# Kernel optimization log

Hardware: AMD Instinct MI355X
Metric: run time of the kernel (lower is better)

## Reference

```python
import jax, jax.numpy as jnp
import numpy as np
from functools import partial

B, S, D, H, DK, DV, DFF = 4, 2048, 1024, 8, 128, 128, 4096
EPS = 1e-6

def rms_norm(x):
    return x * jax.lax.rsqrt(jnp.mean(x * x, axis=-1, keepdims=True) + EPS)

def l2norm(x):
    return x * jax.lax.rsqrt(jnp.sum(x * x, axis=-1, keepdims=True) + EPS)

def setup_inputs() -> dict:
    key = jax.random.key(0)
    ks = jax.random.split(key, 16)
    w = lambda k, shp: jax.random.normal(k, shp, dtype=jnp.float32) * 0.02
    return {
        'x': jax.random.normal(ks[0], (B, S, D), dtype=jnp.float32),
        'Wq': w(ks[1], (D, H * DK)),
        'Wk': w(ks[2], (D, H * DK)),
        'Wv': w(ks[3], (D, H * DV)),
        'Wb': w(ks[4], (D, H)),
        'Wa': w(ks[5], (D, H)),
        'A_log': jnp.log(jnp.linspace(1.0, 8.0, H).astype(jnp.float32)),
        'dt_bias': jax.random.normal(ks[6], (H,), dtype=jnp.float32) * 0.1,
        'Wg': w(ks[7], (D, H * DV)),
        'o_norm_w': jnp.ones((DV,), dtype=jnp.float32),
        'Wo': w(ks[8], (H * DV, D)),
        'W_fc': w(ks[9], (D, DFF)),
        'W_proj': w(ks[10], (DFF, D)),
    }

def gated_delta_net(h, Wq, Wk, Wv, Wb, Wa, A_log, dt_bias, Wg, o_norm_w, Wo):
    b, s, _ = h.shape
    q = l2norm(jax.nn.silu(h @ Wq).reshape(b, s, H, DK))
    k = l2norm(jax.nn.silu(h @ Wk).reshape(b, s, H, DK))
    v = jax.nn.silu(h @ Wv).reshape(b, s, H, DV)
    beta = jax.nn.sigmoid(h @ Wb)                                  # [b,s,H]
    g = -jnp.exp(A_log) * jax.nn.softplus(h @ Wa + dt_bias)       # [b,s,H]
    alpha = jnp.exp(g)
    scale = DK ** -0.5

    # time-major for scan
    tm = lambda a: jnp.moveaxis(a, 1, 0)
    qs, ks_, vs, als, bts = tm(q), tm(k), tm(v), tm(alpha), tm(beta)

    def step(Sst, inp):
        q_t, k_t, v_t, a_t, b_t = inp               # [b,H,dk],[b,H,dk],[b,H,dv],[b,H],[b,H]
        Sst = Sst * a_t[..., None, None]            # decay state [b,H,dk,dv]
        kv = jnp.einsum('bhd,bhde->bhe', k_t, Sst)  # current memory readout
        delta = (v_t - kv) * b_t[..., None]
        Sst = Sst + jnp.einsum('bhd,bhe->bhde', k_t, delta)
        o_t = jnp.einsum('bhd,bhde->bhe', q_t, Sst) * scale
        return Sst, o_t

    S0 = jnp.zeros((b, H, DK, DV), dtype=h.dtype)
    _, o = jax.lax.scan(step, S0, (qs, ks_, vs, als, bts))
    o = jnp.moveaxis(o, 0, 1)                       # [b,s,H,dv]

    gate = (h @ Wg).reshape(b, s, H, DV)
    o = rms_norm(o) * o_norm_w * jax.nn.silu(gate)  # gated RMSNorm
    return o.reshape(b, s, H * DV) @ Wo

def reference(x, Wq, Wk, Wv, Wb, Wa, A_log, dt_bias, Wg, o_norm_w, Wo, W_fc, W_proj):
    ln_scale = 1.0  # config.layer_norm_scaling = False
    h = gated_delta_net(ln_scale * rms_norm(x), Wq, Wk, Wv, Wb, Wa, A_log, dt_bias, Wg, o_norm_w, Wo)
    x = x + h
    m = ln_scale * rms_norm(x)
    y = jnp.square(jax.nn.relu(m @ W_fc)) @ W_proj  # nanoGPT ReLU^2 MLP
    return x + y
```

## Files before the change

kernel.cpp:

```cpp
#include <hip/hip_runtime.h>
#include <math.h>
#include <stdint.h>

#define ROWS 8192
#define DIM  1024
#define NH   8
#define DFF_ 4096
#define EPSF 1e-6f
#define SCALEQ 0.08838834764831845f

typedef __attribute__((ext_vector_type(8))) short short8;
typedef __attribute__((ext_vector_type(4))) float f32x4;

__device__ __forceinline__ float siluf(float x) {
    float e = __expf(-x);
    return x * __builtin_amdgcn_rcpf(1.0f + e);
}
__device__ __forceinline__ unsigned short f2bf(float f) {
    uint32_t u = __float_as_uint(f);
    uint32_t r = (u + 0x7FFFu + ((u >> 16) & 1u)) >> 16;
    return (unsigned short)r;
}
__device__ __forceinline__ float bf2f(unsigned short u) {
    return __uint_as_float(((uint32_t)u) << 16);
}

__device__ __forceinline__ void async16(const void* g, void* l) {
    __builtin_amdgcn_global_load_lds(
        (const __attribute__((address_space(1))) uint32_t*)g,
        (__attribute__((address_space(3))) uint32_t*)l, 16, 0, 0);
}

__global__ void rmsnorm_bf16_kernel(const float* __restrict__ x, unsigned short* __restrict__ y) {
    int row = blockIdx.x;
    int tid = threadIdx.x;
    const float4* x4 = (const float4*)(x + (size_t)row * DIM);
    float4 v = x4[tid];
    float ss = v.x * v.x + v.y * v.y + v.z * v.z + v.w * v.w;
#pragma unroll
    for (int m = 1; m < 64; m <<= 1) ss += __shfl_xor(ss, m, 64);
    __shared__ float wss[4];
    if ((tid & 63) == 0) wss[tid >> 6] = ss;
    __syncthreads();
    float tot = wss[0] + wss[1] + wss[2] + wss[3];
    float r = rsqrtf(tot * (1.0f / 1024.0f) + EPSF);
    ushort4 o;
    o.x = f2bf(v.x * r); o.y = f2bf(v.y * r); o.z = f2bf(v.z * r); o.w = f2bf(v.w * r);
    ((ushort4*)(y + (size_t)row * DIM))[tid] = o;
}

__global__ void transpose_bf16_kernel(const float* __restrict__ W, unsigned short* __restrict__ WT,
                                      int K, int N) {
    __shared__ float tile[32][33];
    int n0 = blockIdx.x * 32, k0 = blockIdx.y * 32;
    int tx = threadIdx.x & 31, ty = threadIdx.x >> 5;
#pragma unroll
    for (int r = 0; r < 32; r += 8)
        tile[ty + r][tx] = W[(size_t)(k0 + ty + r) * N + n0 + tx];
    __syncthreads();
#pragma unroll
    for (int r = 0; r < 32; r += 8)
        WT[(size_t)(n0 + ty + r) * K + k0 + tx] = f2bf(tile[tx][ty + r]);
}

__global__ void transpose5_kernel(const float* __restrict__ s0, const float* __restrict__ s1,
                                  const float* __restrict__ s2, const float* __restrict__ s3,
                                  const float* __restrict__ s4, unsigned short* __restrict__ dst) {
    __shared__ float tile[32][33];
    int z = blockIdx.z;
    const float* W = (z == 0) ? s0 : (z == 1) ? s1 : (z == 2) ? s2 : (z == 3) ? s3 : s4;
    unsigned short* WT = dst + (size_t)z * (1u << 20);
    int n0 = blockIdx.x * 32, k0 = blockIdx.y * 32;
    int tx = threadIdx.x & 31, ty = threadIdx.x >> 5;
#pragma unroll
    for (int r = 0; r < 32; r += 8)
        tile[ty + r][tx] = W[(size_t)(k0 + ty + r) * 1024 + n0 + tx];
    __syncthreads();
#pragma unroll
    for (int r = 0; r < 32; r += 8)
        WT[(size_t)(n0 + ty + r) * 1024 + k0 + tx] = f2bf(tile[tx][ty + r]);
}

#define G256_DECL \
    __shared__ __align__(16) unsigned short AL[2][2][256 * 32]; \
    __shared__ __align__(16) unsigned short BL[2][2][256 * 32]; \
    int tid = threadIdx.x; \
    int w = tid >> 6, lane = tid & 63; \
    int wm = w >> 2, wn = w & 3; \
    int lr = lane & 15; \
    int nwgx = gridDim.x; \
    int nwg = nwgx * gridDim.y; \
    int id = blockIdx.y * nwgx + blockIdx.x; \
    int cpx = nwg >> 3; \
    int nid = (id & 7) * cpx + (id >> 3); \
    int bxs = nid % nwgx, bys = nid / nwgx; \
    int bm = bys * 256, bn = bxs * 256; \
    int stg_r = w * 32 + (lane >> 2); \
    int stg_c = ((lane & 3) ^ ((lane >> 3) & 3)) * 8; \
    const unsigned short* Ag = A + (size_t)(bm + stg_r) * K + stg_c; \
    const unsigned short* Bg = BT + (size_t)(bn + stg_r) * K + stg_c; \
    int pc = ((lane >> 4) ^ ((lr >> 1) & 3)) * 8; \
    f32x4 acc[8][4] = {}; \
    short8 bf[4], af[4]; \
    int nt = K / 64;

#define G256_STAGE_A(buf, s, kto) do { \
    async16(Ag + (kto) + (s) * 32, &AL[buf][s][(w * 2 + 0) * 512]); \
    async16(Ag + (size_t)16 * K + (kto) + (s) * 32, &AL[buf][s][(w * 2 + 1) * 512]); \
} while (0)
#define G256_STAGE_B(buf, s, kto) do { \
    async16(Bg + (kto) + (s) * 32, &BL[buf][s][(w * 2 + 0) * 512]); \
    async16(Bg + (size_t)16 * K + (kto) + (s) * 32, &BL[buf][s][(w * 2 + 1) * 512]); \
} while (0)

#define G256_READ_B(cur, s) do { \
    _Pragma("unroll") \
    for (int j = 0; j < 4; ++j) \
        bf[j] = *(const short8*)&BL[cur][s][(wn * 64 + j * 16 + lr) * 32 + pc]; \
} while (0)
#define G256_READ_A(cur, s, rh) do { \
    _Pragma("unroll") \
    for (int i = 0; i < 4; ++i) \
        af[i] = *(const short8*)&AL[cur][s][(wm * 128 + (rh) * 64 + i * 16 + lr) * 32 + pc]; \
} while (0)

#define G256_MFMA(rh) do { \
    __builtin_amdgcn_s_barrier(); \
    asm volatile("s_waitcnt lgkmcnt(0)" ::: "memory"); \
    __builtin_amdgcn_s_setprio(1); \
    _Pragma("unroll") \
    for (int i = 0; i < 4; ++i) \
        _Pragma("unroll") \
        for (int j = 0; j < 4; ++j) \
            acc[(rh) * 4 + i][j] = __builtin_amdgcn_mfma_f32_16x16x32_bf16(af[i], bf[j], acc[(rh) * 4 + i][j], 0, 0, 0); \
    __builtin_amdgcn_s_setprio(0); \
} while (0)

#define G256_MAINLOOP \
    G256_STAGE_A(0, 0, 0); G256_STAGE_B(0, 0, 0); \
    G256_STAGE_A(0, 1, 0); G256_STAGE_B(0, 1, 0); \
    asm volatile("s_waitcnt vmcnt(0)" ::: "memory"); \
    __builtin_amdgcn_s_barrier(); \
    for (int t = 0; t < nt; ++t) { \
        int cur = t & 1, nxt = cur ^ 1; \
        bool pf = (t + 1 < nt); \
        int ktn = (t + 1) * 64; \
        G256_READ_B(cur, 0); \
        G256_READ_A(cur, 0, 0); \
        if (pf) G256_STAGE_A(nxt, 0, ktn); \
        G256_MFMA(0); \
        __builtin_amdgcn_s_barrier(); \
        G256_READ_A(cur, 0, 1); \
        if (pf) G256_STAGE_B(nxt, 0, ktn); \
        G256_MFMA(1); \
        asm volatile("s_waitcnt vmcnt(4)" ::: "memory"); \
        __builtin_amdgcn_s_barrier(); \
        G256_READ_B(cur, 1); \
        G256_READ_A(cur, 1, 0); \
        if (pf) G256_STAGE_A(nxt, 1, ktn); \
        G256_MFMA(0); \
        __builtin_amdgcn_s_barrier(); \
        G256_READ_A(cur, 1, 1); \
        if (pf) G256_STAGE_B(nxt, 1, ktn); \
        G256_MFMA(1); \
        asm volatile("s_waitcnt vmcnt(4)" ::: "memory"); \
        __builtin_amdgcn_s_barrier(); \
    }

template <int EPI, typename CT>
__global__ __launch_bounds__(512, 2) void gemm256(
    const unsigned short* __restrict__ A, const unsigned short* __restrict__ BT,
    CT* __restrict__ C, const float* __restrict__ res, int M, int N, int K) {
    G256_DECL
    G256_MAINLOOP

#pragma unroll
    for (int rf = 0; rf < 8; ++rf) {
        int gr0 = bm + wm * 128 + rf * 16 + (lane >> 4) * 4;
#pragma unroll
        for (int cf = 0; cf < 4; ++cf) {
            int gc = bn + wn * 64 + cf * 16 + lr;
#pragma unroll
            for (int r = 0; r < 4; ++r) {
                float v = acc[rf][cf][r];
                size_t idx = (size_t)(gr0 + r) * N + gc;
                if (EPI == 2) v += res[idx];
                else if (EPI == 3) { float t = fmaxf(v, 0.0f); v = t * t; }
                if constexpr (sizeof(CT) == 2) C[idx] = (CT)f2bf(v);
                else C[idx] = v;
            }
        }
    }
}

__global__ __launch_bounds__(512, 2) void qkvg256(
    const unsigned short* __restrict__ A, const unsigned short* __restrict__ BT,
    unsigned short* __restrict__ oq, unsigned short* __restrict__ ok,
    unsigned short* __restrict__ ov, unsigned short* __restrict__ og, int M, int K) {
    __shared__ float sums[256 * 4];
    G256_DECL
    G256_MAINLOOP

    int bsel = bn >> 10;
    int bnl = bn & 1023;
    if (bsel < 3) {
#pragma unroll
        for (int rf = 0; rf < 8; ++rf)
#pragma unroll
            for (int cf = 0; cf < 4; ++cf)
#pragma unroll
                for (int r = 0; r < 4; ++r)
                    acc[rf][cf][r] = siluf(acc[rf][cf][r]);
    }
    bool donorm = (bsel < 2);
    if (donorm) {
#pragma unroll
        for (int rf = 0; rf < 8; ++rf) {
#pragma unroll
            for (int r = 0; r < 4; ++r) {
                float p = acc[rf][0][r] * acc[rf][0][r] + acc[rf][1][r] * acc[rf][1][r] +
                          acc[rf][2][r] * acc[rf][2][r] + acc[rf][3][r] * acc[rf][3][r];
                p += __shfl_xor(p, 1, 16);
                p += __shfl_xor(p, 2, 16);
                p += __shfl_xor(p, 4, 16);
                p += __shfl_xor(p, 8, 16);
                if (lr == 0)
                    sums[(wm * 128 + rf * 16 + (lane >> 4) * 4 + r) * 4 + wn] = p;
            }
        }
        __syncthreads();
    }
    unsigned short* C = (bsel == 0) ? oq : (bsel == 1) ? ok : (bsel == 2) ? ov : og;
#pragma unroll
    for (int rf = 0; rf < 8; ++rf) {
#pragma unroll
        for (int r = 0; r < 4; ++r) {
            int lrow = wm * 128 + rf * 16 + (lane >> 4) * 4 + r;
            float rn = 1.0f;
            if (donorm)
                rn = rsqrtf(sums[lrow * 4 + (wn & 2)] + sums[lrow * 4 + (wn & 2) + 1] + EPSF);
            size_t gr = (size_t)(bm + lrow) * 1024;
#pragma unroll
            for (int cf = 0; cf < 4; ++cf) {
                int gc = bnl + wn * 64 + cf * 16 + lr;
                C[gr + gc] = f2bf(acc[rf][cf][r] * rn);
            }
        }
    }
}

template <int EPI>
__global__ __launch_bounds__(512, 2) void gemm128n(
    const unsigned short* __restrict__ A, const unsigned short* __restrict__ BT,
    float* __restrict__ C, const float* __restrict__ res, int M, int N, int K) {
    __shared__ __align__(16) unsigned short AL[2][2][128 * 32];
    __shared__ __align__(16) unsigned short BL[2][2][256 * 32];
    int tid = threadIdx.x;
    int w = tid >> 6, lane = tid & 63;
    int wm = w >> 2, wn = w & 3;
    int lr = lane & 15;
    int nwgx = gridDim.x;
    int nwg = nwgx * gridDim.y;
    int id = blockIdx.y * nwgx + blockIdx.x;
    int cpx = nwg >> 3;
    int nid = (id & 7) * cpx + (id >> 3);
    int bxs = nid % nwgx, bys = nid / nwgx;
    int bm = bys * 128, bn = bxs * 256;
    int stg_r = w * 16 + (lane >> 2);
    int stg_c = ((lane & 3) ^ ((lane >> 3) & 3)) * 8;
    const unsigned short* Ag = A + (size_t)(bm + stg_r) * K + stg_c;
    const unsigned short* Bg = BT + (size_t)(bn + stg_r) * K + stg_c;
    int pc = ((lane >> 4) ^ ((lr >> 1) & 3)) * 8;
    f32x4 acc[4][4] = {};
    short8 bf[4], af[4];
    int nt = K / 64;

#define G128_STAGE_A(buf, s, kto) \
    async16(Ag + (kto) + (s) * 32, &AL[buf][s][w * 512])
#define G128_STAGE_B(buf, s, kto) do { \
    async16(Bg + (kto) + (s) * 32, &BL[buf][s][w * 512]); \
    async16(Bg + (size_t)128 * K + (kto) + (s) * 32, &BL[buf][s][4096 + w * 512]); \
} while (0)
#define G128_READ(cur, s) do { \
    _Pragma("unroll") \
    for (int j = 0; j < 4; ++j) \
        bf[j] = *(const short8*)&BL[cur][s][(wn * 64 + j * 16 + lr) * 32 + pc]; \
    _Pragma("unroll") \
    for (int i = 0; i < 4; ++i) \
        af[i] = *(const short8*)&AL[cur][s][(wm * 64 + i * 16 + lr) * 32 + pc]; \
} while (0)
#define G128_MFMA() do { \
    __builtin_amdgcn_s_barrier(); \
    asm volatile("s_waitcnt lgkmcnt(0)" ::: "memory"); \
    __builtin_amdgcn_s_setprio(1); \
    _Pragma("unroll") \
    for (int i = 0; i < 4; ++i) \
        _Pragma("unroll") \
        for (int j = 0; j < 4; ++j) \
            acc[i][j] = __builtin_amdgcn_mfma_f32_16x16x32_bf16(af[i], bf[j], acc[i][j], 0, 0, 0); \
    __builtin_amdgcn_s_setprio(0); \
} while (0)

    G128_STAGE_A(0, 0, 0); G128_STAGE_B(0, 0, 0);
    G128_STAGE_A(0, 1, 0); G128_STAGE_B(0, 1, 0);
    asm volatile("s_waitcnt vmcnt(0)" ::: "memory");
    __builtin_amdgcn_s_barrier();
    for (int t = 0; t < nt; ++t) {
        int cur = t & 1, nxt = cur ^ 1;
        bool pf = (t + 1 < nt);
        int ktn = (t + 1) * 64;
        G128_READ(cur, 0);
        if (pf) { G128_STAGE_A(nxt, 0, ktn); G128_STAGE_B(nxt, 0, ktn); }
        G128_MFMA();
        asm volatile("s_waitcnt vmcnt(3)" ::: "memory");
        __builtin_amdgcn_s_barrier();
        G128_READ(cur, 1);
        if (pf) { G128_STAGE_A(nxt, 1, ktn); G128_STAGE_B(nxt, 1, ktn); }
        G128_MFMA();
        asm volatile("s_waitcnt vmcnt(3)" ::: "memory");
        __builtin_amdgcn_s_barrier();
    }

#pragma unroll
    for (int i = 0; i < 4; ++i) {
        int gr0 = bm + wm * 64 + i * 16 + (lane >> 4) * 4;
#pragma unroll
        for (int j = 0; j < 4; ++j) {
            int gc = bn + wn * 64 + j * 16 + lr;
#pragma unroll
            for (int r = 0; r < 4; ++r) {
                float v = acc[i][j][r];
                size_t idx = (size_t)(gr0 + r) * N + gc;
                if (EPI == 2) v += res[idx];
                C[idx] = v;
            }
        }
    }
#undef G128_STAGE_A
#undef G128_STAGE_B
#undef G128_READ
#undef G128_MFMA
}

__global__ void gating_kernel(const float* __restrict__ o, const unsigned short* __restrict__ gate,
                              const float* __restrict__ w, unsigned short* __restrict__ ob) {
    int row = blockIdx.x;
    int tid = threadIdx.x;
    const float4* op = (const float4*)(o + (size_t)row * DIM);
    float4 v = op[tid];
    float ss = v.x * v.x + v.y * v.y + v.z * v.z + v.w * v.w;
#pragma unroll
    for (int m = 1; m < 32; m <<= 1) ss += __shfl_xor(ss, m, 32);
    float r = rsqrtf(ss * (1.0f / 128.0f) + EPSF);
    ushort4 gu = ((const ushort4*)(gate + (size_t)row * DIM))[tid];
    float4 wv = ((const float4*)w)[tid & 31];
    ushort4 out;
    out.x = f2bf(v.x * r * wv.x * siluf(bf2f(gu.x)));
    out.y = f2bf(v.y * r * wv.y * siluf(bf2f(gu.y)));
    out.z = f2bf(v.z * r * wv.z * siluf(bf2f(gu.z)));
    out.w = f2bf(v.w * r * wv.w * siluf(bf2f(gu.w)));
    ((ushort4*)(ob + (size_t)row * DIM))[tid] = out;
}

__global__ void smallproj_kernel(const unsigned short* __restrict__ hbuf,
                                 const float* __restrict__ Wb, const float* __restrict__ Wa,
                                 const float* __restrict__ A_log, const float* __restrict__ dt_bias,
                                 float* __restrict__ Glog, float* __restrict__ Beta) {
    int row = blockIdx.x;
    int tid = threadIdx.x;
    __shared__ __align__(16) float hrow[1024];
    __shared__ float part[128];
    const ushort4* h4 = (const ushort4*)(hbuf + (size_t)row * DIM);
    ushort4 u0 = h4[tid * 2], u1 = h4[tid * 2 + 1];
    hrow[tid * 8 + 0] = bf2f(u0.x); hrow[tid * 8 + 1] = bf2f(u0.y);
    hrow[tid * 8 + 2] = bf2f(u0.z); hrow[tid * 8 + 3] = bf2f(u0.w);
    hrow[tid * 8 + 4] = bf2f(u1.x); hrow[tid * 8 + 5] = bf2f(u1.y);
    hrow[tid * 8 + 6] = bf2f(u1.z); hrow[tid * 8 + 7] = bf2f(u1.w);
    __syncthreads();
    int out = tid & 15, slice = tid >> 4;
    const float* W = (out < 8) ? Wb : Wa;
    int col = out & 7;
    int k0 = slice * 128;
    float p = 0.0f;
    for (int kk = 0; kk < 128; kk++) p += hrow[k0 + kk] * W[(size_t)(k0 + kk) * 8 + col];
    part[tid] = p;
    __syncthreads();
    if (tid < 16) {
        float sum = 0.0f;
#pragma unroll
        for (int sl = 0; sl < 8; sl++) sum += part[sl * 16 + tid];
        if (tid < 8) {
            Beta[(size_t)row * 8 + tid] = 1.0f / (1.0f + expf(-sum));
        } else {
            int hh = tid - 8;
            float xg = sum + dt_bias[hh];
            float sp = fmaxf(xg, 0.0f) + log1pf(expf(-fabsf(xg)));
            Glog[(size_t)row * 8 + hh] = -expf(A_log[hh]) * sp;
        }
    }
}

#define PRE_KB 0
#define PRE_QB 17408
#define PRE_YL 17408
#define PRE_LM 34816
#define PRE_MT 44032
#define PRE_FL 76800
#define PRE_SZ 77824

__global__ __launch_bounds__(256) void chunk_prep_kernel(
    const unsigned short* __restrict__ Q16, const unsigned short* __restrict__ K16,
    const unsigned short* __restrict__ V16, const float* __restrict__ Glog,
    const float* __restrict__ Beta,
    unsigned short* __restrict__ Wg, unsigned short* __restrict__ Ug,
    unsigned short* __restrict__ Qg, unsigned short* __restrict__ KTg,
    unsigned short* __restrict__ SMg, float* __restrict__ Pcs) {
    __shared__ __align__(16) unsigned char smem[PRE_SZ];
    unsigned short* Kb = (unsigned short*)(smem + PRE_KB);
    unsigned short* Qb = (unsigned short*)(smem + PRE_QB);
    unsigned short* Yl = (unsigned short*)(smem + PRE_YL);
    unsigned short* Lm = (unsigned short*)(smem + PRE_LM);
    float* betl = (float*)(smem + PRE_FL);
    float* Gl = betl + 64;
    float* Pl = Gl + 64;
    float* decf = Pl + 64;

    int blk = blockIdx.x;
    int bh = blk & 31, c = blk >> 5;
    int b = bh >> 3, h = bh & 7;
    int bhc = bh * 32 + c;
    int row0 = b * 2048 + c * 64;
    int col0 = h * 128;
    int tid = threadIdx.x;
    int wv = tid >> 6, lane = tid & 63;
    int lr = lane & 15, lk8 = (lane >> 4) * 8, l4 = (lane >> 4) * 4;

#pragma unroll
    for (int r = 0; r < 4; ++r) {
        int cc = tid + r * 256;
        int i = cc >> 4, jc = (cc & 15) * 8;
        *(short8*)&Kb[i * 136 + jc] = *(const short8*)(K16 + (size_t)(row0 + i) * DIM + col0 + jc);
        *(short8*)&Qb[i * 136 + jc] = *(const short8*)(Q16 + (size_t)(row0 + i) * DIM + col0 + jc);
    }
    {
        short8 z = {};
        for (int o = tid; o < 576; o += 256) ((short8*)Lm)[o] = z;
        for (int o = tid; o < 2048; o += 256) ((short8*)(smem + PRE_MT))[o] = z;
    }
    if (tid < 64) {
        float g = Glog[(size_t)(row0 + tid) * 8 + h];
        betl[tid] = Beta[(size_t)(row0 + tid) * 8 + h];
#pragma unroll
        for (int d = 1; d < 64; d <<= 1) {
            float t = __shfl_up(g, d, 64);
            if (tid >= d) g += t;
        }
        Gl[tid] = g;
        Pl[tid] = __expf(g);
        float g63 = __shfl(g, 63, 64);
        decf[tid] = __expf(g63 - g);
        if (tid == 63) Pcs[bhc] = __expf(g);
    }
    __syncthreads();

    for (int nt = 0; nt <= wv; nt++) {
        f32x4 acc = {};
#pragma unroll
        for (int kk = 0; kk < 4; kk++) {
            short8 af = *(const short8*)&Kb[(wv * 16 + lr) * 136 + kk * 32 + lk8];
            short8 bfr = *(const short8*)&Kb[(nt * 16 + lr) * 136 + kk * 32 + lk8];
            acc = __builtin_amdgcn_mfma_f32_16x16x32_bf16(af, bfr, acc, 0, 0, 0);
        }
#pragma unroll
        for (int r = 0; r < 4; r++) {
            int i = wv * 16 + l4 + r;
            int j = nt * 16 + lr;
            if (j < i) Lm[i * 72 + j] = f2bf(betl[i] * __expf(Gl[i] - Gl[j]) * acc[r]);
        }
    }
    for (int nt = 0; nt < 4; nt++) {
        f32x4 acc = {};
        if (nt <= wv) {
#pragma unroll
            for (int kk = 0; kk < 4; kk++) {
                short8 af = *(const short8*)&Qb[(wv * 16 + lr) * 136 + kk * 32 + lk8];
                short8 bfr = *(const short8*)&Kb[(nt * 16 + lr) * 136 + kk * 32 + lk8];
                acc = __builtin_amdgcn_mfma_f32_16x16x32_bf16(af, bfr, acc, 0, 0, 0);
            }
        }
#pragma unroll
        for (int r = 0; r < 4; r++) {
            int i = wv * 16 + l4 + r;
            int j = nt * 16 + lr;
            float vv = (nt <= wv && j <= i) ? SCALEQ * __expf(Gl[i] - Gl[j]) * acc[r] : 0.f;
            SMg[((size_t)bhc * 64 + i) * 64 + j] = f2bf(vv);
        }
    }
    {
        int d = tid & 127, ih = tid >> 7;
        for (int i0 = 0; i0 < 32; i0++) {
            int i = ih * 32 + i0;
            Qg[((size_t)bhc * 64 + i) * 128 + d] = f2bf(SCALEQ * Pl[i] * bf2f(Qb[i * 136 + d]));
        }
        for (int j8 = 0; j8 < 32; j8 += 8) {
            short8 v8;
#pragma unroll
            for (int e = 0; e < 8; e++) {
                int jj = ih * 32 + j8 + e;
                v8[e] = (short)f2bf(decf[jj] * bf2f(Kb[jj * 136 + d]));
            }
            *(short8*)&KTg[((size_t)bhc * 128 + d) * 64 + ih * 32 + j8] = v8;
        }
    }
    __syncthreads();

    int n = tid;
    bool isW = n < 128;
    int cW = n & 127;
    unsigned short* Gout = isW ? Wg : Ug;
    const unsigned short* Vcol = V16 + (size_t)row0 * DIM + col0 + cW;
    for (int bi = 0; bi < 4; ++bi) {
        if (bi > 0) {
            int ib = bi * 16;
#pragma unroll
            for (int t4 = 0; t4 < 4; ++t4) {
                int nt = wv * 4 + t4;
                f32x4 acc = {};
#pragma unroll
                for (int ks = 0; ks < 2; ++ks) {
                    short8 af = *(const short8*)&Lm[(ib + lr) * 72 + ks * 32 + lk8];
                    int nr = nt * 16 + lr;
                    int cj = ks * 4 + (lk8 >> 3);
                    short8 bfr = *(const short8*)(smem + PRE_MT + nr * 128 + (((cj ^ (nr & 7)) & 7) << 4));
                    acc = __builtin_amdgcn_mfma_f32_16x16x32_bf16(af, bfr, acc, 0, 0, 0);
                }
#pragma unroll
                for (int r = 0; r < 4; ++r)
                    Yl[(l4 + r) * 264 + nt * 16 + lr] = f2bf(acc[r]);
            }
        }
        __syncthreads();
        float xs[16];
#pragma unroll
        for (int ii = 0; ii < 16; ++ii) {
            int i = bi * 16 + ii;
            float a = isW ? betl[i] * Pl[i] * bf2f(Kb[i * 136 + cW])
                          : betl[i] * bf2f(Vcol[(size_t)i * DIM]);
            if (bi > 0) a -= bf2f(Yl[ii * 264 + n]);
#pragma unroll
            for (int j = 0; j < 15; ++j)
                if (j < ii) a = fmaf(-bf2f(Lm[i * 72 + bi * 16 + j]), xs[j], a);
            xs[ii] = a;
        }
        {
            short8 m0, m1;
#pragma unroll
            for (int e = 0; e < 8; ++e) { m0[e] = (short)f2bf(xs[e]); m1[e] = (short)f2bf(xs[8 + e]); }
            int cj0 = bi * 2, cj1 = bi * 2 + 1;
            *(short8*)(smem + PRE_MT + n * 128 + (((cj0 ^ (n & 7)) & 7) << 4)) = m0;
            *(short8*)(smem + PRE_MT + n * 128 + (((cj1 ^ (n & 7)) & 7) << 4)) = m1;
        }
#pragma unroll
        for (int ii = 0; ii < 16; ++ii)
            Gout[((size_t)bhc * 64 + bi * 16 + ii) * 128 + cW] = f2bf(xs[ii]);
        __syncthreads();
    }
}

__global__ __launch_bounds__(256) void chunk_scan2_kernel(
    const unsigned short* __restrict__ Wg, const unsigned short* __restrict__ Ug,
    const unsigned short* __restrict__ Qg, const unsigned short* __restrict__ KTg,
    const unsigned short* __restrict__ SMg, const float* __restrict__ Pcs,
    float* __restrict__ O) {
    int blk = blockIdx.x;
    int bh = blk & 31, dvg = blk >> 5;
    int b = bh >> 3, h = bh & 7;
    int col16 = dvg * 16;
    int tid = threadIdx.x;
    int wv = tid >> 6, lane = tid & 63;
    int lr = lane & 15, lk8 = (lane >> 4) * 8, l4 = (lane >> 4) * 4;
    int i0 = wv * 16;

    __shared__ __align__(16) unsigned short Wl[64 * 136];
    __shared__ __align__(16) unsigned short Ql[64 * 136];
    __shared__ __align__(16) unsigned short KTl[128 * 72];
    __shared__ __align__(16) unsigned short SMl[64 * 72];
    __shared__ __align__(16) unsigned short Ul[64 * 24];
    __shared__ __align__(16) unsigned short STl[16 * 136];
    __shared__ __align__(16) unsigned short DTl[16 * 72];

    for (int e = tid; e < 16 * 136; e += 256) STl[e] = 0;

    f32x4 Sacc[2] = {};

    for (int c = 0; c < 32; c++) {
        int bhc = bh * 32 + c;
        size_t base8k = (size_t)bhc * 8192;
        float pc = Pcs[bhc];
#pragma unroll
        for (int r = 0; r < 4; r++) {
            int v = tid + r * 256;
            *(short8*)&Wl[(v >> 4) * 136 + (v & 15) * 8] = *(const short8*)(Wg + base8k + (size_t)v * 8);
            *(short8*)&Ql[(v >> 4) * 136 + (v & 15) * 8] = *(const short8*)(Qg + base8k + (size_t)v * 8);
            *(short8*)&KTl[(v >> 3) * 72 + (v & 7) * 8] = *(const short8*)(KTg + base8k + (size_t)v * 8);
        }
#pragma unroll
        for (int r = 0; r < 2; r++) {
            int v = tid + r * 256;
            *(short8*)&SMl[(v >> 3) * 72 + (v & 7) * 8] = *(const short8*)(SMg + (size_t)bhc * 4096 + (size_t)v * 8);
        }
        if (tid < 128) {
            int row = tid >> 1, hf = tid & 1;
            *(short8*)&Ul[row * 24 + hf * 8] =
                *(const short8*)(Ug + base8k + (size_t)row * 128 + col16 + hf * 8);
        }
        __syncthreads();

        f32x4 acc0 = {}, acc1 = {};
#pragma unroll
        for (int kd = 0; kd < 4; kd++) {
            short8 bfs = *(const short8*)&STl[lr * 136 + kd * 32 + lk8];
            short8 aw = *(const short8*)&Wl[(i0 + lr) * 136 + kd * 32 + lk8];
            short8 aq = *(const short8*)&Ql[(i0 + lr) * 136 + kd * 32 + lk8];
            acc0 = __builtin_amdgcn_mfma_f32_16x16x32_bf16(aw, bfs, acc0, 0, 0, 0);
            acc1 = __builtin_amdgcn_mfma_f32_16x16x32_bf16(aq, bfs, acc1, 0, 0, 0);
        }
        ushort4 dpk;
        dpk.x = f2bf(bf2f(Ul[(i0 + l4 + 0) * 24 + lr]) - acc0[0]);
        dpk.y = f2bf(bf2f(Ul[(i0 + l4 + 1) * 24 + lr]) - acc0[1]);
        dpk.z = f2bf(bf2f(Ul[(i0 + l4 + 2) * 24 + lr]) - acc0[2]);
        dpk.w = f2bf(bf2f(Ul[(i0 + l4 + 3) * 24 + lr]) - acc0[3]);
        *(ushort4*)&DTl[lr * 72 + i0 + l4] = dpk;
        __syncthreads();

#pragma unroll
        for (int dt = 0; dt < 2; dt++)
#pragma unroll
            for (int r = 0; r < 4; r++) Sacc[dt][r] *= pc;
#pragma unroll
        for (int kj = 0; kj < 2; kj++) {
            short8 bfd = *(const short8*)&DTl[lr * 72 + kj * 32 + lk8];
            short8 as = *(const short8*)&SMl[(i0 + lr) * 72 + kj * 32 + lk8];
            acc1 = __builtin_amdgcn_mfma_f32_16x16x32_bf16(as, bfd, acc1, 0, 0, 0);
#pragma unroll
            for (int dt = 0; dt < 2; dt++) {
                short8 ak = *(const short8*)&KTl[((2 * wv + dt) * 16 + lr) * 72 + kj * 32 + lk8];
                Sacc[dt] = __builtin_amdgcn_mfma_f32_16x16x32_bf16(ak, bfd, Sacc[dt], 0, 0, 0);
            }
        }
        {
            int orow0 = b * 2048 + c * 64 + i0 + l4;
            int ocol = h * 128 + col16 + lr;
#pragma unroll
            for (int r = 0; r < 4; r++)
                O[(size_t)(orow0 + r) * DIM + ocol] = acc1[r];
        }
#pragma unroll
        for (int dt = 0; dt < 2; dt++) {
            ushort4 sp;
            sp.x = f2bf(Sacc[dt][0]);
            sp.y = f2bf(Sacc[dt][1]);
            sp.z = f2bf(Sacc[dt][2]);
            sp.w = f2bf(Sacc[dt][3]);
            *(ushort4*)&STl[lr * 136 + (2 * wv + dt) * 16 + l4] = sp;
        }
        __syncthreads();
    }
}

extern "C" void kernel_launch(void* const* d_in, const int* in_sizes, int n_in,
                              void* d_out, int out_size, void* d_ws, size_t ws_size,
                              hipStream_t stream) {
    const float* x      = (const float*)d_in[0];
    const float* Wq     = (const float*)d_in[1];
    const float* Wk     = (const float*)d_in[2];
    const float* Wv     = (const float*)d_in[3];
    const float* Wb     = (const float*)d_in[4];
    const float* Wa     = (const float*)d_in[5];
    const float* A_log  = (const float*)d_in[6];
    const float* dt_b   = (const float*)d_in[7];
    const float* Wg_in  = (const float*)d_in[8];
    const float* o_norm = (const float*)d_in[9];
    const float* Wo     = (const float*)d_in[10];
    const float* W_fc   = (const float*)d_in[11];
    const float* W_proj = (const float*)d_in[12];
    float* out = (float*)d_out;

    const size_t MATE = (size_t)ROWS * DIM;
    unsigned short* qb16 = (unsigned short*)d_ws;
    unsigned short* kb16 = qb16 + MATE;
    unsigned short* vb16 = kb16 + MATE;
    unsigned short* gt16 = vb16 + MATE;
    float* o_f = (float*)(gt16 + MATE);
    unsigned short* h_bf = (unsigned short*)(o_f + MATE);
    float* glog = (float*)(h_bf + MATE);
    float* beta = glog + (size_t)ROWS * NH;
    unsigned short* wts = (unsigned short*)(beta + (size_t)ROWS * NH);
    unsigned short* WqT = wts;
    unsigned short* WoT = wts + 4 * (1u << 20);
    unsigned short* WfcT = wts + 5 * (1u << 20);
    unsigned short* WprT = wts + 9 * (1u << 20);
    unsigned short* Wgb = wts + 13 * (1u << 20);
    unsigned short* Ugb = Wgb + (8u << 20);
    unsigned short* Qg2 = Ugb + (8u << 20);
    unsigned short* KTg = Qg2 + (8u << 20);
    unsigned short* SMg = KTg + (8u << 20);
    float* pcs = (float*)(SMg + (4u << 20));
    unsigned short* m_bf = h_bf;
    unsigned short* o_bf = vb16;
    unsigned short* fc_bf = qb16;

    transpose5_kernel<<<dim3(32, 32, 5), 256, 0, stream>>>(Wq, Wk, Wv, Wg_in, Wo, WqT);
    transpose_bf16_kernel<<<dim3(128, 32), 256, 0, stream>>>(W_fc, WfcT, 1024, 4096);
    transpose_bf16_kernel<<<dim3(32, 128), 256, 0, stream>>>(W_proj, WprT, 4096, 1024);

    rmsnorm_bf16_kernel<<<ROWS, 256, 0, stream>>>(x, h_bf);

    qkvg256<<<dim3(4096 / 256, ROWS / 256), 512, 0, stream>>>(
        h_bf, WqT, qb16, kb16, vb16, gt16, ROWS, DIM);

    smallproj_kernel<<<ROWS, 128, 0, stream>>>(h_bf, Wb, Wa, A_log, dt_b, glog, beta);

    chunk_prep_kernel<<<1024, 256, 0, stream>>>(qb16, kb16, vb16, glog, beta,
                                                Wgb, Ugb, Qg2, KTg, SMg, pcs);
    chunk_scan2_kernel<<<256, 256, 0, stream>>>(Wgb, Ugb, Qg2, KTg, SMg, pcs, o_f);

    gating_kernel<<<ROWS, 256, 0, stream>>>(o_f, gt16, o_norm, o_bf);

    gemm128n<2><<<dim3(1024 / 256, ROWS / 128), 512, 0, stream>>>(
        o_bf, WoT, out, x, ROWS, DIM, DIM);

    rmsnorm_bf16_kernel<<<ROWS, 256, 0, stream>>>(out, m_bf);

    gemm256<3, unsigned short><<<dim3(DFF_ / 256, ROWS / 256), 512, 0, stream>>>(
        m_bf, WfcT, fc_bf, nullptr, ROWS, DFF_, DIM);

    gemm128n<2><<<dim3(1024 / 256, ROWS / 128), 512, 0, stream>>>(
        fc_bf, WprT, out, out, ROWS, DIM, DFF_);
}
```

Baseline: 486.5 us.

## Restructure gemm128n pipeline to one barrier per 64-wide K tile

Reorganizes the gemm128n shared-memory layout from two 32-wide K sub-stages to a single 64-wide row with XOR swizzle over 8 chunks. Each iteration now issues all prefetch loads for the next tile, reads both K halves of fragments, and runs 32 MFMAs before a single wait and barrier. This cuts barrier and wait count per K tile and gives more MFMA work between syncs. The price is more fragment registers. The launch bound also drops the 2-blocks-per-CU hint, which may lower occupancy.

```diff
diff --git a/kernel.cpp b/kernel.cpp
--- a/kernel.cpp
+++ b/kernel.cpp
@@ -250,11 +250,11 @@
 }
 
 template <int EPI>
-__global__ __launch_bounds__(512, 2) void gemm128n(
+__global__ __launch_bounds__(512) void gemm128n(
     const unsigned short* __restrict__ A, const unsigned short* __restrict__ BT,
     float* __restrict__ C, const float* __restrict__ res, int M, int N, int K) {
-    __shared__ __align__(16) unsigned short AL[2][2][128 * 32];
-    __shared__ __align__(16) unsigned short BL[2][2][256 * 32];
+    __shared__ __align__(16) unsigned short AL[2][128 * 64];
+    __shared__ __align__(16) unsigned short BL[2][256 * 64];
     int tid = threadIdx.x;
     int w = tid >> 6, lane = tid & 63;
     int wm = w >> 2, wn = w & 3;
@@ -266,60 +266,62 @@
     int nid = (id & 7) * cpx + (id >> 3);
     int bxs = nid % nwgx, bys = nid / nwgx;
     int bm = bys * 128, bn = bxs * 256;
-    int stg_r = w * 16 + (lane >> 2);
-    int stg_c = ((lane & 3) ^ ((lane >> 3) & 3)) * 8;
-    const unsigned short* Ag = A + (size_t)(bm + stg_r) * K + stg_c;
-    const unsigned short* Bg = BT + (size_t)(bn + stg_r) * K + stg_c;
-    int pc = ((lane >> 4) ^ ((lr >> 1) & 3)) * 8;
+
+    int arow = tid >> 3;
+    int ac = ((tid & 7) ^ (arow & 7)) * 8;
+    const unsigned short* Aga = A + (size_t)(bm + arow) * K + ac;
+    const unsigned short* Bga = BT + (size_t)(bn + arow) * K + ac;
+
+    int pc0 = ((0 * 4 + (lane >> 4)) ^ (lr & 7)) * 8;
+    int pc1 = ((1 * 4 + (lane >> 4)) ^ (lr & 7)) * 8;
+
     f32x4 acc[4][4] = {};
-    short8 bf[4], af[4];
+    short8 af0[4], af1[4], bf0[4], bf1[4];
     int nt = K / 64;
 
-#define G128_STAGE_A(buf, s, kto) \
-    async16(Ag + (kto) + (s) * 32, &AL[buf][s][w * 512])
-#define G128_STAGE_B(buf, s, kto) do { \
-    async16(Bg + (kto) + (s) * 32, &BL[buf][s][w * 512]); \
-    async16(Bg + (size_t)128 * K + (kto) + (s) * 32, &BL[buf][s][4096 + w * 512]); \
+#define G128_STAGE(buf, kto) do { \
+    async16(Aga + (kto), &AL[buf][tid * 8]); \
+    async16(Aga + (size_t)64 * K + (kto), &AL[buf][(512 + tid) * 8]); \
+    async16(Bga + (kto), &BL[buf][tid * 8]); \
+    async16(Bga + (size_t)64 * K + (kto), &BL[buf][(512 + tid) * 8]); \
+    async16(Bga + (size_t)128 * K + (kto), &BL[buf][(1024 + tid) * 8]); \
+    async16(Bga + (size_t)192 * K + (kto), &BL[buf][(1536 + tid) * 8]); \
 } while (0)
-#define G128_READ(cur, s) do { \
-    _Pragma("unroll") \
-    for (int j = 0; j < 4; ++j) \
-        bf[j] = *(const short8*)&BL[cur][s][(wn * 64 + j * 16 + lr) * 32 + pc]; \
-    _Pragma("unroll") \
-    for (int i = 0; i < 4; ++i) \
-        af[i] = *(const short8*)&AL[cur][s][(wm * 64 + i * 16 + lr) * 32 + pc]; \
-} while (0)
-#define G128_MFMA() do { \
-    __builtin_amdgcn_s_barrier(); \
-    asm volatile("s_waitcnt lgkmcnt(0)" ::: "memory"); \
-    __builtin_amdgcn_s_setprio(1); \
-    _Pragma("unroll") \
-    for (int i = 0; i < 4; ++i) \
-        _Pragma("unroll") \
-        for (int j = 0; j < 4; ++j) \
-            acc[i][j] = __builtin_amdgcn_mfma_f32_16x16x32_bf16(af[i], bf[j], acc[i][j], 0, 0, 0); \
-    __builtin_amdgcn_s_setprio(0); \
-} while (0)
-
-    G128_STAGE_A(0, 0, 0); G128_STAGE_B(0, 0, 0);
-    G128_STAGE_A(0, 1, 0); G128_STAGE_B(0, 1, 0);
+
+    G128_STAGE(0, 0);
     asm volatile("s_waitcnt vmcnt(0)" ::: "memory");
     __builtin_amdgcn_s_barrier();
     for (int t = 0; t < nt; ++t) {
         int cur = t & 1, nxt = cur ^ 1;
-        bool pf = (t + 1 < nt);
-        int ktn = (t + 1) * 64;
-        G128_READ(cur, 0);
-        if (pf) { G128_STAGE_A(nxt, 0, ktn); G128_STAGE_B(nxt, 0, ktn); }
-        G128_MFMA();
-        asm volatile("s_waitcnt vmcnt(3)" ::: "memory");
+        if (t + 1 < nt) G128_STAGE(nxt, (t + 1) * 64);
+#pragma unroll
+        for (int i = 0; i < 4; ++i) {
+            af0[i] = *(const short8*)&AL[cur][(wm * 64 + i * 16 + lr) * 64 + pc0];
+            af1[i] = *(const short8*)&AL[cur][(wm * 64 + i * 16 + lr) * 64 + pc1];
+        }
+#pragma unroll
+        for (int j = 0; j < 4; ++j) {
+            bf0[j] = *(const short8*)&BL[cur][(wn * 64 + j * 16 + lr) * 64 + pc0];
+            bf1[j] = *(const short8*)&BL[cur][(wn * 64 + j * 16 + lr) * 64 + pc1];
+        }
+        asm volatile("s_waitcnt lgkmcnt(0)" ::: "memory");
+        __builtin_amdgcn_sched_barrier(0);
+        __builtin_amdgcn_s_setprio(1);
+#pragma unroll
+        for (int i = 0; i < 4; ++i)
+#pragma unroll
+            for (int j = 0; j < 4; ++j)
+                acc[i][j] = __builtin_amdgcn_mfma_f32_16x16x32_bf16(af0[i], bf0[j], acc[i][j], 0, 0, 0);
+#pragma unroll
+        for (int i = 0; i < 4; ++i)
+#pragma unroll
+            for (int j = 0; j < 4; ++j)
+                acc[i][j] = __builtin_amdgcn_mfma_f32_16x16x32_bf16(af1[i], bf1[j], acc[i][j], 0, 0, 0);
+        __builtin_amdgcn_s_setprio(0);
+        asm volatile("s_waitcnt vmcnt(0)" ::: "memory");
         __builtin_amdgcn_s_barrier();
-        G128_READ(cur, 1);
-        if (pf) { G128_STAGE_A(nxt, 1, ktn); G128_STAGE_B(nxt, 1, ktn); }
-        G128_MFMA();
-        asm volatile("s_waitcnt vmcnt(3)" ::: "memory");
-        __builtin_amdgcn_s_barrier();
-    }
+    }
+#undef G128_STAGE
 
 #pragma unroll
     for (int i = 0; i < 4; ++i) {
@@ -336,10 +338,6 @@
             }
         }
     }
-#undef G128_STAGE_A
-#undef G128_STAGE_B
-#undef G128_READ
-#undef G128_MFMA
 }
 
 __global__ void gating_kernel(const float* __restrict__ o, const unsigned short* __restrict__ gate,
```

Result: no change. 492.1 us (+1.1%).
